# Optimization experiments

Measured on AMD Instinct MI355X. Metric: run time of the kernel, lower is better.

## Reference

```python
import jax, jax.numpy as jnp
import numpy as np

WS = 8          # window size
NH = 16         # num heads
EPS = 1e-6      # LinearAttention eps

def _rel_pos_index(ws):
    coords = np.stack(np.meshgrid(np.arange(ws), np.arange(ws), indexing='ij'))
    cf = coords.reshape(2, -1)
    rel = (cf[:, :, None] - cf[:, None, :]).transpose(1, 2, 0).astype(np.int64)
    rel[:, :, 0] += ws - 1
    rel[:, :, 1] += ws - 1
    rel[:, :, 0] *= 2 * ws - 1
    return rel.sum(-1)

REL_IDX = _rel_pos_index(WS)  # (ws*ws, ws*ws) int index into bias table

def conv1x1(x, w, b=None):
    y = jnp.einsum('bchw,oc->bohw', x, w)
    return y if b is None else y + b[None, :, None, None]

def conv3x3(x, w):
    return jax.lax.conv_general_dilated(x, w, (1, 1), [(1, 1), (1, 1)],
        dimension_numbers=('NCHW', 'OIHW', 'NCHW'))

def dwconv(x, w, pad):
    return jax.lax.conv_general_dilated(x, w, (1, 1), [(pad, pad), (pad, pad)],
        dimension_numbers=('NCHW', 'OIHW', 'NCHW'), feature_group_count=x.shape[1])

def bn(x, scale, bias):
    # eval-mode BatchNorm folded to per-channel affine (running_mean=0, running_var=1)
    return x * scale[None, :, None, None] + bias[None, :, None, None]

def rpad(x, l, r, t, b):
    return jnp.pad(x, ((0, 0), (0, 0), (t, b), (l, r)), mode='reflect')

def avgpool(x, kh, kw, ph, pw):
    # torch AvgPool2d with zero padding, count_include_pad=True
    xp = jnp.pad(x, ((0, 0), (0, 0), (ph, ph), (pw, pw)))
    s = jax.lax.reduce_window(xp, 0.0, jax.lax.add, (1, 1, kh, kw), (1, 1, 1, 1), 'VALID')
    return s / (kh * kw)

def linear_attention(x, gamma, wq, bq, wk, bk, wv, bv):
    B, C, H, W = x.shape
    N = H * W
    Q = conv1x1(x, wq, bq).reshape(B, -1, N)   # (B, M, N), M = C // 8
    K = conv1x1(x, wk, bk).reshape(B, -1, N)
    V = conv1x1(x, wv, bv).reshape(B, C, N)
    Q = Q / jnp.linalg.norm(Q, axis=-2, keepdims=True)  # l2_norm over channel dim
    K = K / jnp.linalg.norm(K, axis=-2, keepdims=True)
    tailor = 1.0 / (N + jnp.einsum('bmn,bm->bn', Q, K.sum(-1) + EPS))  # (B, N)
    vsum = V.sum(-1)                                    # (B, C)
    matrix = jnp.einsum('bmn,bcn->bmc', K, V)           # (B, M, C)
    msum = vsum[:, :, None] + jnp.einsum('bmn,bmc->bcn', Q, matrix)    # (B, C, N)
    return x + gamma * (msum * tailor[:, None, :]).reshape(B, C, H, W)

def fusion_attention(x, y, wqkv, wl1, s1, b1, wl2, s2, b2, rel, wdw, sp, bp, wpw):
    B, C, H, W = x.shape  # H, W divisible by WS -> pad() branch is a no-op
    local = bn(conv1x1(y, wl2), s2, b2) + bn(conv3x3(y, wl1), s1, b1)
    d = C // NH
    qkv = conv1x1(x, wqkv)                              # (B, 3C, H, W)
    hh, ww = H // WS, W // WS
    t = qkv.reshape(B, 3, NH, d, hh, WS, ww, WS)
    t = t.transpose(1, 0, 4, 6, 2, 5, 7, 3).reshape(3, B * hh * ww, NH, WS * WS, d)
    q, k, v = t[0], t[1], t[2]
    dots = jnp.einsum('wnqd,wnkd->wnqk', q, k) * (d ** -0.5)
    bias = rel[REL_IDX.reshape(-1)].reshape(WS * WS, WS * WS, NH).transpose(2, 0, 1)
    attn = jax.nn.softmax(dots + bias[None], axis=-1)
    out = jnp.einsum('wnqk,wnkd->wnqd', attn, v)
    out = out.reshape(B, hh, ww, NH, WS, WS, d).transpose(0, 3, 6, 1, 4, 2, 5).reshape(B, C, H, W)
    out = (avgpool(rpad(out, 0, 0, 0, 1), WS, 1, WS // 2 - 1, 0)
           + avgpool(rpad(out, 0, 1, 0, 0), 1, WS, 0, WS // 2 - 1))
    out = out + local
    out = rpad(out, 0, 1, 0, 1)                          # pad_out
    out = conv1x1(bn(dwconv(out, wdw, (WS - 1) // 2), sp, bp), wpw)  # SeparableConvBN
    return out[:, :, :H, :W]

def setup_inputs() -> dict:
    key = jax.random.key(0)
    ks = jax.random.split(key, 24)
    B, C, H, W = 2, 256, 256, 256
    M = C // 8
    n = jax.random.normal
    inp = {
        'x': n(ks[0], (B, C, H, W), jnp.float32),
        'y': n(ks[1], (B, C, H, W), jnp.float32),
        'la_gamma': jnp.float32(0.5),
        'la_wq': n(ks[2], (M, C)) * 0.05, 'la_bq': n(ks[3], (M,)) * 0.02,
        'la_wk': n(ks[4], (M, C)) * 0.05, 'la_bk': n(ks[5], (M,)) * 0.02,
        'la_wv': n(ks[6], (C, C)) * 0.05, 'la_bv': n(ks[7], (C,)) * 0.02,
        'fa_wqkv': n(ks[8], (3 * C, C)) * 0.05,
        'fa_wl1': n(ks[9], (C, C, 3, 3)) * 0.02,
        'fa_s1': 1.0 + n(ks[10], (C,)) * 0.02, 'fa_b1': n(ks[11], (C,)) * 0.02,
        'fa_wl2': n(ks[12], (C, C)) * 0.05,
        'fa_s2': 1.0 + n(ks[13], (C,)) * 0.02, 'fa_b2': n(ks[14], (C,)) * 0.02,
        'fa_rel': n(ks[15], ((2 * WS - 1) ** 2, NH)) * 0.02,
        'fa_wdw': n(ks[16], (C, 1, WS, WS)) * 0.05,
        'fa_sp': 1.0 + n(ks[17], (C,)) * 0.02, 'fa_bp': n(ks[18], (C,)) * 0.02,
        'fa_wpw': n(ks[19], (C, C)) * 0.05,
    }
    return inp

def reference(x, y, la_gamma, la_wq, la_bq, la_wk, la_bk, la_wv, la_bv,
              fa_wqkv, fa_wl1, fa_s1, fa_b1, fa_wl2, fa_s2, fa_b2,
              fa_rel, fa_wdw, fa_sp, fa_bp, fa_wpw):
    z = linear_attention(x, la_gamma, la_wq, la_bq, la_wk, la_bk, la_wv, la_bv)
    return fusion_attention(z, y, fa_wqkv, fa_wl1, fa_s1, fa_b1, fa_wl2, fa_s2, fa_b2,
                            fa_rel, fa_wdw, fa_sp, fa_bp, fa_wpw)
```

## Files before the change

kernel.cpp:

```cpp
#include <hip/hip_runtime.h>
#include <hip/hip_bf16.h>

#define DI __device__ __forceinline__

constexpr int Bc = 2, Cc = 256, Hc = 256, Wc = 256, Nc = Hc * Wc;
constexpr float LA_EPS = 1e-6f;

typedef __attribute__((ext_vector_type(8))) short short8;
typedef __attribute__((ext_vector_type(4))) float floatx4;
typedef __attribute__((ext_vector_type(16))) float floatx16;

union Frag { short8 v; uint u[4]; };

DI ushort f2bf(float f) {
    uint u = __float_as_uint(f);
    uint r = (u + 0x7fff + ((u >> 16) & 1)) >> 16;
    return (ushort)r;
}

DI float bf2f(ushort u) { return __uint_as_float((uint)u << 16); }

DI uint pack2(float a, float b) {
    return (uint)f2bf(a) | ((uint)f2bf(b) << 16);
}

DI void gload16(const void* g, void* l) {
    __builtin_amdgcn_global_load_lds(
        (const __attribute__((address_space(1))) void*)g,
        (__attribute__((address_space(3))) void*)l, 16, 0, 0);
}

__global__ __launch_bounds__(256) void kprep_x(const float* __restrict__ x,
        ushort* __restrict__ xbf)
{
    int blk = blockIdx.x;
    int b = blk >> 13;
    int rest = blk & 8191;
    int ci0 = (rest & 7) * 32;
    int n0 = (rest >> 3) * 64;
    int t = threadIdx.x;
    __shared__ uint u[16][65];
    int px = t & 63, cig = t >> 6;
    const float* yb = x + (((size_t)(b * 256 + ci0 + cig * 8)) << 16) + n0 + px;
    #pragma unroll
    for (int jj = 0; jj < 4; ++jj) {
        float v0 = yb[((size_t)(jj * 2)) << 16];
        float v1 = yb[((size_t)(jj * 2 + 1)) << 16];
        u[cig * 4 + jj][px] = pack2(v0, v1);
    }
    __syncthreads();
    uint* out32 = (uint*)xbf;
    int pr = t & 15, pg = t >> 4;
    #pragma unroll
    for (int g2 = 0; g2 < 4; ++g2) {
        int ppx = g2 * 16 + pg;
        size_t uidx = (((size_t)(b * 65536 + n0 + ppx) * 256 + ci0) >> 1) + pr;
        out32[uidx] = u[pr][ppx];
    }
}

__global__ __launch_bounds__(256) void kprep_qk(const float* __restrict__ wq,
        const float* __restrict__ wk, ushort* __restrict__ Wqkb)
{
    int idx = blockIdx.x * 256 + threadIdx.x;
    int oc = idx >> 8, ci = idx & 255;
    float v = (oc < 32) ? wq[oc * 256 + ci] : wk[(oc - 32) * 256 + ci];
    Wqkb[idx] = f2bf(v);
}

__global__ __launch_bounds__(512, 2) void k1_mfma(
        const ushort* __restrict__ xbf, const ushort* __restrict__ Wqkb,
        const float* __restrict__ bq, const float* __restrict__ bk,
        float* __restrict__ Qo, float* __restrict__ Ko)
{
    int blk = blockIdx.x;
    int b = blk >> 10;
    int px0 = (blk & 1023) << 6;
    int t = threadIdx.x;
    int lane = t & 63, w = t >> 6;
    int wr = w >> 2;
    int wc = w & 3;

    __shared__ ushort sW[64 * 256];
    __shared__ ushort sX[64 * 256];

    #pragma unroll
    for (int p = 0; p < 4; ++p) {
        int m = p * 512 + t;
        int row = m >> 5, ch = m & 31;
        const ushort* g = Wqkb + row * 256 + ((ch ^ (row & 7)) << 3);
        gload16(g, (char*)sW + p * 8192 + w * 1024);
    }
    const ushort* xb = xbf + (size_t)(b * 65536 + px0) * 256;
    #pragma unroll
    for (int p = 0; p < 4; ++p) {
        int m = p * 512 + t;
        int row = m >> 5, ch = m & 31;
        const ushort* g = xb + row * 256 + ((ch ^ (row & 7)) << 3);
        gload16(g, (char*)sX + p * 8192 + w * 1024);
    }
    __syncthreads();

    int l15 = lane & 15, l4 = lane >> 4;
    floatx4 acc[2];
    acc[0] = {0.f, 0.f, 0.f, 0.f};
    acc[1] = {0.f, 0.f, 0.f, 0.f};

    #pragma unroll
    for (int ks = 0; ks < 8; ++ks) {
        int cidx = ks * 4 + l4;
        short8 af[2];
        #pragma unroll
        for (int m2 = 0; m2 < 2; ++m2) {
            int row = wr * 32 + m2 * 16 + l15;
            af[m2] = *(const short8*)((const char*)sW + row * 512 + ((cidx ^ (row & 7)) << 4));
        }
        int brow = wc * 16 + l15;
        short8 bf_ = *(const short8*)((const char*)sX + brow * 512 + ((cidx ^ (brow & 7)) << 4));
        #pragma unroll
        for (int m2 = 0; m2 < 2; ++m2)
            acc[m2] = __builtin_amdgcn_mfma_f32_16x16x32_bf16(af[m2], bf_, acc[m2], 0, 0, 0);
    }

    const float* bias = wr ? bk : bq;
    float* outp = wr ? Ko : Qo;
    float v[2][4];
    float s = 0.f;
    #pragma unroll
    for (int m2 = 0; m2 < 2; ++m2)
        #pragma unroll
        for (int r = 0; r < 4; ++r) {
            float vv = acc[m2][r] + bias[m2 * 16 + l4 * 4 + r];
            v[m2][r] = vv;
            s += vv * vv;
        }
    s += __shfl_xor(s, 16);
    s += __shfl_xor(s, 32);
    float rn = rsqrtf(s);
    int px = px0 + wc * 16 + l15;
    #pragma unroll
    for (int m2 = 0; m2 < 2; ++m2)
        #pragma unroll
        for (int r = 0; r < 4; ++r) {
            int oc = m2 * 16 + l4 * 4 + r;
            outp[((size_t)(b * 32 + oc) << 16) + px] = v[m2][r] * rn;
        }
}

__global__ __launch_bounds__(256) void k2_kx(const ushort* __restrict__ xbf,
        const float* __restrict__ Kn, float* __restrict__ KXp,
        float* __restrict__ xsp, float* __restrict__ ksp)
{
    int blk = blockIdx.x;
    int b = blk >> 9;
    int blkl = blk & 511;
    int t = threadIdx.x;
    int n0 = blkl * 128;
    __shared__ float kT[32][128];
    for (int i = t; i < 4096; i += 256) {
        int m = i >> 7, p = i & 127;
        kT[m][p] = Kn[((size_t)(b * 32 + m) << 16) + n0 + p];
    }
    __syncthreads();
    float acc[32];
    #pragma unroll
    for (int m = 0; m < 32; ++m) acc[m] = 0.f;
    float xs = 0.f;
    const ushort* xb = xbf + (((size_t)(b * 65536 + n0)) << 8) + t;
    for (int p4 = 0; p4 < 32; ++p4) {
        float xv0 = bf2f(xb[(size_t)(p4 * 4 + 0) << 8]);
        float xv1 = bf2f(xb[(size_t)(p4 * 4 + 1) << 8]);
        float xv2 = bf2f(xb[(size_t)(p4 * 4 + 2) << 8]);
        float xv3 = bf2f(xb[(size_t)(p4 * 4 + 3) << 8]);
        xs += xv0 + xv1 + xv2 + xv3;
        #pragma unroll
        for (int m = 0; m < 32; ++m) {
            floatx4 kv = *(const floatx4*)&kT[m][p4 * 4];
            acc[m] += kv[0] * xv0 + kv[1] * xv1 + kv[2] * xv2 + kv[3] * xv3;
        }
    }
    xsp[blk * 256 + t] = xs;
    if (t < 32) {
        float ks = 0.f;
        for (int p = 0; p < 128; ++p) ks += kT[t][p];
        ksp[blk * 32 + t] = ks;
    }
    #pragma unroll
    for (int m = 0; m < 32; ++m) KXp[(size_t)blk * 8192 + m * 256 + t] = acc[m];
}

__global__ __launch_bounds__(256) void k2r(const float* __restrict__ KXp,
        const float* __restrict__ xsp, const float* __restrict__ ksp,
        float* __restrict__ KX, float* __restrict__ xsum, float* __restrict__ Ksum)
{
    int blk = blockIdx.x, t = threadIdx.x;
    if (blk < 64) {
        int gidx = blk * 256 + t;
        int b = gidx >> 13, idx = gidx & 8191;
        float s = 0.f;
        for (int ch = 0; ch < 512; ++ch)
            s += KXp[(size_t)((b << 9) + ch) * 8192 + idx];
        KX[gidx] = s;
    } else if (blk < 66) {
        int b = blk - 64;
        float s = 0.f;
        for (int ch = 0; ch < 512; ++ch)
            s += xsp[((b << 9) + ch) * 256 + t];
        xsum[b * 256 + t] = s;
    } else {
        int b = blk - 66;
        if (t < 32) {
            float s = 0.f;
            for (int ch = 0; ch < 512; ++ch)
                s += ksp[((b << 9) + ch) * 32 + t];
            Ksum[b * 32 + t] = s;
        }
    }
}

__global__ __launch_bounds__(256) void k3_mat(const float* __restrict__ wv,
        const float* __restrict__ bv, const float* __restrict__ KX,
        const float* __restrict__ xsum, const float* __restrict__ Ksum,
        float* __restrict__ matrix, float* __restrict__ vsum)
{
    int b = blockIdx.x, t = threadIdx.x;
    __shared__ float sx[256];
    __shared__ float sk[32];
    __shared__ float skx[32][256];
    __shared__ float wT[256][65];
    sx[t] = xsum[b * 256 + t];
    if (t < 32) sk[t] = Ksum[b * 32 + t];
    for (int j = 0; j < 32; ++j) skx[j][t] = KX[(b * 32 + j) * 256 + t];
    float vs = bv[t] * (float)Nc;
    float mv[32];
    #pragma unroll
    for (int m = 0; m < 32; ++m) mv[m] = 0.f;
    for (int cc0 = 0; cc0 < 256; cc0 += 64) {
        __syncthreads();
        for (int i = 0; i < 64; ++i) {
            int c = i * 4 + (t >> 6);
            wT[c][t & 63] = wv[(size_t)c * 256 + cc0 + (t & 63)];
        }
        __syncthreads();
        for (int ccl = 0; ccl < 64; ++ccl) {
            float w = wT[t][ccl];
            int cc = cc0 + ccl;
            vs += w * sx[cc];
            #pragma unroll
            for (int m = 0; m < 32; ++m) mv[m] += w * skx[m][cc];
        }
    }
    vsum[b * 256 + t] = vs;
    float bvt = bv[t];
    for (int m = 0; m < 32; ++m) matrix[(b * 32 + m) * 256 + t] = mv[m] + bvt * sk[m];
}

__global__ __launch_bounds__(256) void k4_z(const float* __restrict__ x,
        const float* __restrict__ Q, const float* __restrict__ matrix,
        const float* __restrict__ vsum, const float* __restrict__ Ksum,
        const float* __restrict__ gamma_p, ushort* __restrict__ zbf)
{
    int b = blockIdx.x >> 10;
    int n0 = (blockIdx.x & 1023) * 64;
    int t = threadIdx.x;
    int px = t & 63, g = t >> 6;
    __shared__ float qT[32][64];
    __shared__ float mat[32][256];
    __shared__ float vs[256];
    __shared__ float tail[64];
    __shared__ float sk[32];
    __shared__ uint zsh[64 * 128];
    #pragma unroll
    for (int j = 0; j < 8; ++j) {
        int m = j * 4 + g;
        qT[m][px] = Q[((size_t)b * 32 + m) * Nc + n0 + px];
    }
    for (int j = 0; j < 32; ++j) {
        int idx = j * 256 + t;
        (&mat[0][0])[idx] = matrix[b * 8192 + idx];
    }
    vs[t] = vsum[b * 256 + t];
    if (t < 32) sk[t] = Ksum[b * 32 + t] + LA_EPS;
    __syncthreads();
    if (t < 64) {
        float s = 0.f;
        #pragma unroll
        for (int m = 0; m < 32; ++m) s += qT[m][t] * sk[m];
        tail[t] = 1.0f / ((float)Nc + s);
    }
    __syncthreads();
    float gamma = gamma_p[0];
    float tl = tail[px];
    for (int l = 0; l < 64; l += 2) {
        int c0 = g * 64 + l;
        float s0 = vs[c0], s1 = vs[c0 + 1];
        #pragma unroll
        for (int m = 0; m < 32; ++m) {
            float qv = qT[m][px];
            s0 += qv * mat[m][c0];
            s1 += qv * mat[m][c0 + 1];
        }
        size_t idx0 = (size_t)(b * 256 + c0) * Nc + n0 + px;
        float z0 = x[idx0] + gamma * s0 * tl;
        float z1 = x[idx0 + Nc] + gamma * s1 * tl;
        int cp = c0 >> 1;
        zsh[(px * 512 + (((cp >> 2) ^ (px & 7)) << 4) + (cp & 3) * 4) >> 2] = pack2(z0, z1);
    }
    __syncthreads();
    const uint4* zl = (const uint4*)zsh;
    uint4* gz = (uint4*)(zbf + (((size_t)(b * 65536 + n0)) << 8));
    #pragma unroll
    for (int i2 = 0; i2 < 8; ++i2)
        gz[i2 * 256 + t] = zl[i2 * 256 + t];
}

__global__ __launch_bounds__(256) void kprep_y(const float* __restrict__ y,
        ushort* __restrict__ ybf)
{
    int blk = blockIdx.x;
    int b = blk >> 13;
    int rest = blk & 8191;
    int ci0 = (rest & 7) * 32;
    int n0 = (rest >> 3) * 64;
    int row = n0 >> 8, x = n0 & 255;
    int t = threadIdx.x;
    __shared__ uint u[16][65];
    int px = t & 63, cig = t >> 6;
    const float* yb = y + (((size_t)(b * 256 + ci0 + cig * 8)) << 16) + n0 + px;
    #pragma unroll
    for (int jj = 0; jj < 4; ++jj) {
        float v0 = yb[((size_t)(jj * 2)) << 16];
        float v1 = yb[((size_t)(jj * 2 + 1)) << 16];
        u[cig * 4 + jj][px] = pack2(v0, v1);
    }
    __syncthreads();
    uint* out32 = (uint*)ybf;
    size_t pbase = (size_t)(row + 1) * 258 + (x + 1);
    int pr = t & 15, pg = t >> 4;
    #pragma unroll
    for (int g2 = 0; g2 < 4; ++g2) {
        int ppx = g2 * 16 + pg;
        size_t uidx = (((size_t)b * 258 * 258 * 256 + (pbase + ppx) * 256 + ci0) >> 1) + pr;
        out32[uidx] = u[pr][ppx];
    }
}

__global__ __launch_bounds__(256) void kprep_w(const float* __restrict__ wl1,
        const float* __restrict__ s1, const float* __restrict__ wl2,
        const float* __restrict__ s2, ushort* __restrict__ Wb)
{
    int idx = blockIdx.x * 256 + threadIdx.x;
    int tp = idx >> 16;
    int r = idx & 65535;
    int co = r >> 8;
    float v = wl1[(size_t)r * 9 + tp] * s1[co];
    if (tp == 4) v += wl2[r] * s2[co];
    Wb[idx] = f2bf(v);
}

__global__ __launch_bounds__(256) void kprep_qw(const float* __restrict__ wqkv,
        ushort* __restrict__ Wqb)
{
    int idx = blockIdx.x * 256 + threadIdx.x;
    float v = wqkv[idx];
    if (idx < 65536) v *= 0.25f;
    Wqb[idx] = f2bf(v);
}

__global__ __launch_bounds__(256) void kprep_pw(const float* __restrict__ wpw,
        ushort* __restrict__ Wpwb)
{
    int idx = blockIdx.x * 256 + threadIdx.x;
    Wpwb[idx] = f2bf(wpw[idx]);
}

__global__ __launch_bounds__(256) void kprep_rel(const float* __restrict__ rel,
        ushort* __restrict__ relbf)
{
    int idx = blockIdx.x * 256 + threadIdx.x;
    if (idx < 3600) {
        int d = idx >> 4, h = idx & 15;
        relbf[h * 226 + d] = f2bf(rel[idx]);
    }
}

__global__ __launch_bounds__(512, 2) void k5_mfma(
        const ushort* __restrict__ ybf, const ushort* __restrict__ Wb,
        const float* __restrict__ b1, const float* __restrict__ b2,
        ushort* __restrict__ L)
{
    int blk = blockIdx.x;
    int b = blk >> 9;
    int y0 = (blk >> 1) & 255;
    int x0 = (blk & 1) << 7;
    int t = threadIdx.x;
    int lane = t & 63;
    int w = t >> 6;
    int wr = w >> 1;
    int wc = w & 1;

    __shared__ ushort sW[256 * 64];
    __shared__ ushort sY[128 * 64];

    floatx4 acc[4][4];
    #pragma unroll
    for (int m = 0; m < 4; ++m)
        #pragma unroll
        for (int n = 0; n < 4; ++n)
            acc[m][n] = {0.f, 0.f, 0.f, 0.f};

    const ushort* yb = ybf + (size_t)b * 258 * 258 * 256;
    int ldsWbase = w * 64 * 16;
    int ldsYbase = w * 64 * 16;

    for (int tp = 0; tp < 9; ++tp) {
        int dy = tp / 3 - 1, dx = tp % 3 - 1;
        const ushort* yrow = yb + ((size_t)(y0 + dy + 1) * 258 + (x0 + dx + 1)) * 256;
        const ushort* wtap = Wb + tp * 65536;
        for (int cb = 0; cb < 4; ++cb) {
            int ci0 = cb * 64;
            __syncthreads();
            #pragma unroll
            for (int p = 0; p < 4; ++p) {
                int m = p * 512 + t;
                int row = m >> 3, ch = m & 7;
                const ushort* g = wtap + row * 256 + ci0 + ((ch ^ (row & 7)) << 3);
                gload16(g, (char*)sW + p * 512 * 16 + ldsWbase);
            }
            #pragma unroll
            for (int p = 0; p < 2; ++p) {
                int m = p * 512 + t;
                int pxr = m >> 3, ch = m & 7;
                const ushort* g = yrow + (size_t)pxr * 256 + ci0 + ((ch ^ (pxr & 7)) << 3);
                gload16(g, (char*)sY + p * 512 * 16 + ldsYbase);
            }
            __syncthreads();
            #pragma unroll
            for (int kk = 0; kk < 2; ++kk) {
                int chunkb = kk * 4 + (lane >> 4);
                short8 afr[4];
                #pragma unroll
                for (int m2 = 0; m2 < 4; ++m2) {
                    int row = wr * 64 + m2 * 16 + (lane & 15);
                    int ch = chunkb ^ (row & 7);
                    afr[m2] = *(const short8*)((const char*)sW + row * 128 + ch * 16);
                }
                #pragma unroll
                for (int n2 = 0; n2 < 4; ++n2) {
                    int row = wc * 64 + n2 * 16 + (lane & 15);
                    int ch = chunkb ^ (row & 7);
                    short8 bfr = *(const short8*)((const char*)sY + row * 128 + ch * 16);
                    #pragma unroll
                    for (int m2 = 0; m2 < 4; ++m2)
                        acc[m2][n2] = __builtin_amdgcn_mfma_f32_16x16x32_bf16(
                            afr[m2], bfr, acc[m2][n2], 0, 0, 0);
                }
            }
        }
    }
    int pxb = x0 + wc * 64 + (lane & 15);
    #pragma unroll
    for (int m2 = 0; m2 < 4; ++m2) {
        int cobase = wr * 64 + m2 * 16 + (lane >> 4) * 4;
        #pragma unroll
        for (int r = 0; r < 4; ++r) {
            int co = cobase + r;
            float bias = b1[co] + b2[co];
            ushort* dst = L + (((size_t)(b * 256 + co)) << 16) + y0 * 256 + pxb;
            #pragma unroll
            for (int n2 = 0; n2 < 4; ++n2)
                dst[n2 * 16] = f2bf(acc[m2][n2][r] + bias);
        }
    }
}

__global__ __launch_bounds__(512, 2) void k6_mfma(const ushort* __restrict__ zbf,
        const ushort* __restrict__ Wqb, const ushort* __restrict__ relbf,
        float* __restrict__ A)
{
    int blk = blockIdx.x;
    int wxp = blk & 15, wy = (blk >> 4) & 31, b = blk >> 9;
    int t = threadIdx.x;
    int lane = t & 63;
    int w = t >> 6;
    int win = w >> 2;
    int wq4 = w & 3;

    __shared__ ushort zT[128 * 256];
    __shared__ ushort srel[16 * 226];

    char* zTc = (char*)zT;

    {
        const ushort* zb = zbf + (((size_t)b) << 16) * 256;
        #pragma unroll
        for (int p = 0; p < 8; ++p) {
            int m = p * 512 + t;
            int row = m >> 5, ch = m & 31;
            int win2 = row >> 6, px = row & 63;
            int gy = wy * 8 + (px >> 3);
            int gx = (wxp * 2 + win2) * 8 + (px & 7);
            const ushort* g = zb + (((size_t)(gy * 256 + gx)) << 8) + ch * 8;
            gload16(g, zTc + p * 8192 + w * 1024);
        }
    }
    for (int i = t; i < 16 * 226; i += 512) srel[i] = relbf[i];
    __syncthreads();

    int l15 = lane & 15, l4 = lane >> 4;
    int l31 = lane & 31, l5 = lane >> 5;
    bool hilane = (l5 != 0);
    bool hi16 = (l31 & 16) != 0;
    int srcA = (l5 << 5) + (l31 & 15);
    int srcB = srcA + 16;
    int pxbase = win * 64;

    for (int hrep = 0; hrep < 4; ++hrep) {
        int h = wq4 * 4 + hrep;
        const ushort* srh = &srel[h * 226];

        floatx4 qacc[4] = {}, kacc[4] = {}, vacc[4] = {};
        #pragma unroll
        for (int ks = 0; ks < 8; ++ks) {
            short8 awq = *(const short8*)(Wqb + ((h * 16 + l15) << 8) + ks * 32 + (l4 << 3));
            short8 awk = *(const short8*)(Wqb + ((256 + h * 16 + l15) << 8) + ks * 32 + (l4 << 3));
            short8 bwv = *(const short8*)(Wqb + ((512 + h * 16 + l15) << 8) + ks * 32 + (l4 << 3));
            #pragma unroll
            for (int n = 0; n < 4; ++n) {
                int px = n * 16 + l15;
                short8 bz = *(const short8*)(zTc + (pxbase + px) * 512 + (((ks * 4 + l4) ^ (px & 7)) << 4));
                qacc[n] = __builtin_amdgcn_mfma_f32_16x16x32_bf16(awq, bz, qacc[n], 0, 0, 0);
                kacc[n] = __builtin_amdgcn_mfma_f32_16x16x32_bf16(awk, bz, kacc[n], 0, 0, 0);
                vacc[n] = __builtin_amdgcn_mfma_f32_16x16x32_bf16(bz, bwv, vacc[n], 0, 0, 0);
            }
        }

        Frag bq[2];
        {
            uint plo[4], phi[4];
            #pragma unroll
            for (int n = 0; n < 4; ++n) {
                plo[n] = pack2(qacc[n][0], qacc[n][1]);
                phi[n] = pack2(qacc[n][2], qacc[n][3]);
            }
            #pragma unroll
            for (int it = 0; it < 2; ++it) {
                uint a0 = (uint)__shfl((int)plo[it * 2], srcA), a1 = (uint)__shfl((int)plo[it * 2 + 1], srcA);
                uint b0 = (uint)__shfl((int)phi[it * 2], srcA), b1 = (uint)__shfl((int)phi[it * 2 + 1], srcA);
                uint c0 = (uint)__shfl((int)plo[it * 2], srcB), c1 = (uint)__shfl((int)plo[it * 2 + 1], srcB);
                uint d0 = (uint)__shfl((int)phi[it * 2], srcB), d1 = (uint)__shfl((int)phi[it * 2 + 1], srcB);
                bq[it].u[0] = hi16 ? a1 : a0;
                bq[it].u[1] = hi16 ? b1 : b0;
                bq[it].u[2] = hi16 ? c1 : c0;
                bq[it].u[3] = hi16 ? d1 : d0;
            }
        }
        Frag ak[2];
        {
            uint plo[4], phi[4];
            #pragma unroll
            for (int n = 0; n < 4; ++n) {
                plo[n] = pack2(kacc[n][0], kacc[n][1]);
                phi[n] = pack2(kacc[n][2], kacc[n][3]);
            }
            #pragma unroll
            for (int jt = 0; jt < 2; ++jt) {
                uint a0 = (uint)__shfl((int)plo[jt * 2], srcA), a1 = (uint)__shfl((int)plo[jt * 2 + 1], srcA);
                uint b0 = (uint)__shfl((int)phi[jt * 2], srcA), b1 = (uint)__shfl((int)phi[jt * 2 + 1], srcA);
                uint c0 = (uint)__shfl((int)plo[jt * 2], srcB), c1 = (uint)__shfl((int)plo[jt * 2 + 1], srcB);
                uint d0 = (uint)__shfl((int)phi[jt * 2], srcB), d1 = (uint)__shfl((int)phi[jt * 2 + 1], srcB);
                ak[jt].u[0] = hi16 ? a1 : a0;
                ak[jt].u[1] = hi16 ? b1 : b0;
                ak[jt].u[2] = hi16 ? c1 : c0;
                ak[jt].u[3] = hi16 ? d1 : d0;
            }
        }
        Frag av[4];
        {
            uint v01[4], v23[4];
            #pragma unroll
            for (int m = 0; m < 4; ++m) {
                v01[m] = pack2(vacc[m][0], vacc[m][1]);
                v23[m] = pack2(vacc[m][2], vacc[m][3]);
            }
            #pragma unroll
            for (int jc = 0; jc < 4; ++jc) {
                av[jc].u[0] = (uint)__shfl((int)v01[jc], srcA);
                av[jc].u[1] = (uint)__shfl((int)v23[jc], srcA);
                av[jc].u[2] = (uint)__shfl((int)v01[jc], srcB);
                av[jc].u[3] = (uint)__shfl((int)v23[jc], srcB);
            }
        }

        #pragma unroll
        for (int it = 0; it < 2; ++it) {
            floatx16 st[2];
            #pragma unroll
            for (int jt = 0; jt < 2; ++jt) {
                floatx16 zc = {};
                st[jt] = __builtin_amdgcn_mfma_f32_32x32x16_bf16(ak[jt].v, bq[it].v, zc, 0, 0, 0);
            }
            int i = it * 32 + l31;
            int Ai = (i >> 3) * 15 + (i & 7) + 112;
            float mx = -1e30f;
            #pragma unroll
            for (int jt = 0; jt < 2; ++jt)
                #pragma unroll
                for (int r = 0; r < 16; ++r) {
                    int j = jt * 32 + (r & 3) + 8 * (r >> 2) + 4 * l5;
                    int Bjr = (j >> 3) * 15 + (j & 7);
                    float s = st[jt][r] + bf2f(srh[Ai - Bjr]);
                    st[jt][r] = s;
                    mx = fmaxf(mx, s);
                }
            mx = fmaxf(mx, __shfl_xor(mx, 32));
            float sum = 0.f;
            #pragma unroll
            for (int jt = 0; jt < 2; ++jt)
                #pragma unroll
                for (int r = 0; r < 16; ++r) {
                    float e = __expf(st[jt][r] - mx);
                    st[jt][r] = e;
                    sum += e;
                }
            sum += __shfl_xor(sum, 32);
            float rinv = 1.0f / sum;

            floatx16 ot = {};
            #pragma unroll
            for (int jc = 0; jc < 4; ++jc) {
                int jt = jc >> 1, rb = (jc & 1) * 8;
                uint u0 = pack2(st[jt][rb + 0], st[jt][rb + 1]);
                uint u1 = pack2(st[jt][rb + 2], st[jt][rb + 3]);
                uint u2 = pack2(st[jt][rb + 4], st[jt][rb + 5]);
                uint u3 = pack2(st[jt][rb + 6], st[jt][rb + 7]);
                uint s0 = (uint)__shfl_xor((int)u0, 32);
                uint s1 = (uint)__shfl_xor((int)u1, 32);
                uint s2 = (uint)__shfl_xor((int)u2, 32);
                uint s3 = (uint)__shfl_xor((int)u3, 32);
                Frag bf;
                bf.u[0] = hilane ? s2 : u0;
                bf.u[1] = hilane ? s3 : u1;
                bf.u[2] = hilane ? u2 : s0;
                bf.u[3] = hilane ? u3 : s1;
                ot = __builtin_amdgcn_mfma_f32_32x32x16_bf16(av[jc].v, bf.v, ot, 0, 0, 0);
            }
            int gy = wy * 8 + (i >> 3);
            int gx = (wxp * 2 + win) * 8 + (i & 7);
            float* Ab = A + (((size_t)(b * 256 + h * 16)) << 16) + gy * 256 + gx;
            #pragma unroll
            for (int r = 0; r < 8; ++r) {
                int d = (r & 3) + 8 * (r >> 2) + 4 * l5;
                Ab[(size_t)d << 16] = ot[r] * rinv;
            }
        }
    }
}

__global__ __launch_bounds__(256) void k7_pool(const float* __restrict__ A,
        ushort* __restrict__ L)
{
    int blk = blockIdx.x;
    int tile = blk & 15;
    int c = (blk >> 4) & 255;
    int b = blk >> 12;
    int ty = (tile >> 2) * 64, tx = (tile & 3) * 64;
    int t = threadIdx.x;
    __shared__ float aT[71][73];
    const float* Ac = A + ((size_t)(b * 256 + c) << 16);
    for (int i = t; i < 71 * 71; i += 256) {
        int rr = i / 71, cc = i - rr * 71;
        int gy = ty + rr - 3, gx = tx + cc - 3;
        float v = 0.f;
        if (gy >= 0 && gy <= 256 && gx >= 0 && gx <= 256) {
            int ry = (gy == 256) ? 254 : gy;
            int rx = (gx == 256) ? 254 : gx;
            v = Ac[ry * 256 + rx];
        }
        aT[rr][cc] = v;
    }
    __syncthreads();
    int jj = t & 63;
    int oy0 = (t >> 6) * 16;
    ushort* Lc = L + ((size_t)(b * 256 + c) << 16);
    #pragma unroll 4
    for (int dy = 0; dy < 16; ++dy) {
        int oi = oy0 + dy;
        float sv = 0.f, sh = 0.f;
        #pragma unroll
        for (int u = 0; u < 8; ++u) {
            sv += aT[oi + u][jj + 3];
            sh += aT[oi + 3][jj + u];
        }
        int idx = (ty + oi) * 256 + tx + jj;
        Lc[idx] = f2bf(bf2f(Lc[idx]) + 0.125f * (sv + sh));
    }
}

__global__ __launch_bounds__(256) void k8_dw(const ushort* __restrict__ P,
        const float* __restrict__ wdw, const float* __restrict__ sp,
        const float* __restrict__ bp, ushort* __restrict__ D)
{
    int blk = blockIdx.x;
    int tile = blk & 63;
    int c = (blk >> 6) & 255;
    int b = blk >> 14;
    int ty = (tile >> 3) * 32, tx = (tile & 7) * 32;
    int t = threadIdx.x;
    __shared__ float pT[39][40];
    __shared__ float wT[64];
    const ushort* Pc = P + ((size_t)(b * 256 + c) << 16);
    for (int i = t; i < 39 * 40; i += 256) {
        int rr = i / 40, cc = i - rr * 40;
        int gy = ty + rr - 3, gx = tx + cc - 3;
        float v = 0.f;
        if (gy >= 0 && gy <= 256 && gx >= 0 && gx <= 256) {
            int ry = (gy == 256) ? 254 : gy;
            int rx = (gx == 256) ? 254 : gx;
            v = bf2f(Pc[ry * 256 + rx]);
        }
        pT[rr][cc] = v;
    }
    if (t < 64) wT[t] = wdw[c * 64 + t];
    __syncthreads();
    int jj = t & 31;
    int oy0 = (t >> 5) * 4;
    float acc[4] = {0.f, 0.f, 0.f, 0.f};
    #pragma unroll
    for (int r = 0; r < 11; ++r) {
        float pv[8];
        #pragma unroll
        for (int v = 0; v < 8; ++v) pv[v] = pT[oy0 + r][jj + v];
        #pragma unroll
        for (int dy = 0; dy < 4; ++dy) {
            if (dy >= r - 7 && dy <= r && dy <= 3) {
                int u = r - dy;
                #pragma unroll
                for (int v = 0; v < 8; ++v)
                    acc[dy] += wT[u * 8 + v] * pv[v];
            }
        }
    }
    float spc = sp[c], bpc = bp[c];
    ushort* Dc = D + ((size_t)(b * 256 + c) << 16);
    #pragma unroll
    for (int dy = 0; dy < 4; ++dy)
        Dc[(ty + oy0 + dy) * 256 + tx + jj] = f2bf(spc * acc[dy] + bpc);
}

__global__ __launch_bounds__(512, 2) void k9_mfma(
        const ushort* __restrict__ D, const ushort* __restrict__ Wpwb,
        float* __restrict__ out)
{
    int blk = blockIdx.x;
    int b = blk >> 9;
    int px0 = (blk & 511) << 7;
    int t = threadIdx.x;
    int lane = t & 63;
    int w = t >> 6;
    int wr = w >> 1, wc = w & 1;

    __shared__ ushort sW[256 * 64];
    __shared__ ushort sD[128 * 64];

    floatx4 acc[4][4];
    #pragma unroll
    for (int m = 0; m < 4; ++m)
        #pragma unroll
        for (int n = 0; n < 4; ++n)
            acc[m][n] = {0.f, 0.f, 0.f, 0.f};

    int ldsWbase = w * 64 * 16;

    for (int cb = 0; cb < 4; ++cb) {
        int ci0 = cb * 64;
        __syncthreads();
        #pragma unroll
        for (int p = 0; p < 4; ++p) {
            int m = p * 512 + t;
            int row = m >> 3, ch = m & 7;
            const ushort* g = Wpwb + row * 256 + ci0 + ((ch ^ (row & 7)) << 3);
            gload16(g, (char*)sW + p * 512 * 16 + ldsWbase);
        }
        #pragma unroll
        for (int p = 0; p < 2; ++p) {
            int m = p * 512 + t;
            int ci = m & 63, pxb = (m >> 6) * 8;
            short8 v = *(const short8*)(D + ((size_t)(b * 256 + ci0 + ci) << 16) + px0 + pxb);
            #pragma unroll
            for (int k2 = 0; k2 < 8; ++k2) {
                int px = pxb + k2;
                *(ushort*)((char*)sD + px * 128 + (((ci >> 3) ^ (px & 7)) << 4) + (ci & 7) * 2) =
                    (ushort)v[k2];
            }
        }
        __syncthreads();
        #pragma unroll
        for (int kk = 0; kk < 2; ++kk) {
            int chunkb = kk * 4 + (lane >> 4);
            short8 afr[4];
            #pragma unroll
            for (int m2 = 0; m2 < 4; ++m2) {
                int row = wr * 64 + m2 * 16 + (lane & 15);
                int ch = chunkb ^ (row & 7);
                afr[m2] = *(const short8*)((const char*)sW + row * 128 + ch * 16);
            }
            #pragma unroll
            for (int n2 = 0; n2 < 4; ++n2) {
                int row = wc * 64 + n2 * 16 + (lane & 15);
                int ch = chunkb ^ (row & 7);
                short8 bfr = *(const short8*)((const char*)sD + row * 128 + ch * 16);
                #pragma unroll
                for (int m2 = 0; m2 < 4; ++m2)
                    acc[m2][n2] = __builtin_amdgcn_mfma_f32_16x16x32_bf16(
                        afr[m2], bfr, acc[m2][n2], 0, 0, 0);
            }
        }
    }
    int pxb = px0 + wc * 64 + (lane & 15);
    #pragma unroll
    for (int m2 = 0; m2 < 4; ++m2) {
        int cobase = wr * 64 + m2 * 16 + (lane >> 4) * 4;
        #pragma unroll
        for (int r = 0; r < 4; ++r) {
            int co = cobase + r;
            float* dst = out + (((size_t)(b * 256 + co)) << 16) + pxb;
            #pragma unroll
            for (int n2 = 0; n2 < 4; ++n2)
                dst[n2 * 16] = acc[m2][n2][r];
        }
    }
}

extern "C" void kernel_launch(void* const* d_in, const int* in_sizes, int n_in,
                              void* d_out, int out_size, void* d_ws, size_t ws_size,
                              hipStream_t stream)
{
    (void)in_sizes; (void)n_in; (void)out_size; (void)ws_size;
    const float* x     = (const float*)d_in[0];
    const float* y     = (const float*)d_in[1];
    const float* gamma = (const float*)d_in[2];
    const float* la_wq = (const float*)d_in[3];
    const float* la_bq = (const float*)d_in[4];
    const float* la_wk = (const float*)d_in[5];
    const float* la_bk = (const float*)d_in[6];
    const float* la_wv = (const float*)d_in[7];
    const float* la_bv = (const float*)d_in[8];
    const float* wqkv  = (const float*)d_in[9];
    const float* wl1   = (const float*)d_in[10];
    const float* s1    = (const float*)d_in[11];
    const float* b1    = (const float*)d_in[12];
    const float* wl2   = (const float*)d_in[13];
    const float* s2    = (const float*)d_in[14];
    const float* b2    = (const float*)d_in[15];
    const float* rel   = (const float*)d_in[16];
    const float* wdw   = (const float*)d_in[17];
    const float* sp    = (const float*)d_in[18];
    const float* bp    = (const float*)d_in[19];
    const float* wpw   = (const float*)d_in[20];
    float* out = (float*)d_out;

    float* ws = (float*)d_ws;
    float* Q      = ws;
    float* Kn     = ws + 4194304;
    float* stats  = ws + 8388608;
    float* Ksum   = stats;
    float* xsum   = stats + 64;
    float* KX     = stats + 576;
    float* matrix = stats + 16960;
    float* vsum   = stats + 33344;
    float* A      = ws + 8429568;
    float* L      = A + 33554432;

    float* KXp   = L;
    float* xsp   = L + 8388608;
    float* ksp   = L + 8650752;
    ushort* xbf  = (ushort*)(L + 8683520);
    ushort* Wqkb = (ushort*)(L + 25460736);

    ushort* Wb    = (ushort*)Kn;
    ushort* Wqb   = (ushort*)Kn + 600064;
    ushort* Wpwb  = (ushort*)Kn + 798720;
    ushort* relbf = (ushort*)Kn + 864256;
    ushort* ybf   = (ushort*)A;
    ushort* Dbf   = (ushort*)A;
    ushort* zbf   = (ushort*)d_out;
    ushort* Lb    = (ushort*)L;

    hipMemsetAsync(ybf, 0, (size_t)2 * 258 * 258 * 256 * sizeof(ushort), stream);

    kprep_y  <<<16384, 256, 0, stream>>>(y, ybf);
    kprep_x  <<<16384, 256, 0, stream>>>(x, xbf);
    kprep_qk <<<64,    256, 0, stream>>>(la_wq, la_wk, Wqkb);
    k1_mfma  <<<2048,  512, 0, stream>>>(xbf, Wqkb, la_bq, la_bk, Q, Kn);
    k2_kx    <<<1024,  256, 0, stream>>>(xbf, Kn, KXp, xsp, ksp);
    kprep_w  <<<2304,  256, 0, stream>>>(wl1, s1, wl2, s2, Wb);
    kprep_qw <<<768,   256, 0, stream>>>(wqkv, Wqb);
    kprep_pw <<<256,   256, 0, stream>>>(wpw, Wpwb);
    kprep_rel<<<15,    256, 0, stream>>>(rel, relbf);
    k2r      <<<68,    256, 0, stream>>>(KXp, xsp, ksp, KX, xsum, Ksum);
    k3_mat   <<<2,     256, 0, stream>>>(la_wv, la_bv, KX, xsum, Ksum, matrix, vsum);
    k4_z     <<<2048,  256, 0, stream>>>(x, Q, matrix, vsum, Ksum, gamma, zbf);
    k5_mfma  <<<1024,  512, 0, stream>>>(ybf, Wb, b1, b2, Lb);
    k6_mfma  <<<1024,  512, 0, stream>>>(zbf, Wqb, relbf, A);
    k7_pool  <<<8192,  256, 0, stream>>>(A, Lb);
    k8_dw    <<<32768, 256, 0, stream>>>(Lb, wdw, sp, bp, Dbf);
    k9_mfma  <<<1024,  512, 0, stream>>>(Dbf, Wpwb, out);
}
```

Before: 1.046 ms.

## Fuse strip-pool add and depthwise conv into one tiled kernel

Merges the pooling kernel, which added the strip average pool of the attention output into the bf16 local tensor, with the depthwise 8x8 conv kernel. Each 64x64 tile now loads a haloed attention tile, computes the pooled-plus-local values for a 74x74 halo region in shared memory, and runs the depthwise conv from there. This removes the bf16 round-trip write and reread of the intermediate and one launch. In exchange it recomputes pooling on halo pixels, uses much more shared memory per block (lower occupancy), and keeps 16 accumulators per thread. The output buffer moves to a separate region.

```diff
diff --git a/kernel.cpp b/kernel.cpp
--- a/kernel.cpp
+++ b/kernel.cpp
@@ -657,8 +657,10 @@
     }
 }
 
-__global__ __launch_bounds__(256) void k7_pool(const float* __restrict__ A,
-        ushort* __restrict__ L)
+__global__ __launch_bounds__(256) void k78_pooldw(const float* __restrict__ A,
+        const ushort* __restrict__ Lc, const float* __restrict__ wdw,
+        const float* __restrict__ sp, const float* __restrict__ bp,
+        ushort* __restrict__ D)
 {
     int blk = blockIdx.x;
     int tile = blk & 15;
@@ -666,75 +668,62 @@
     int b = blk >> 12;
     int ty = (tile >> 2) * 64, tx = (tile & 3) * 64;
     int t = threadIdx.x;
-    __shared__ float aT[71][73];
+
+    __shared__ float aT[81][84];
+    __shared__ float lT[74][76];
+    __shared__ float wT[64];
+
     const float* Ac = A + ((size_t)(b * 256 + c) << 16);
-    for (int i = t; i < 71 * 71; i += 256) {
-        int rr = i / 71, cc = i - rr * 71;
-        int gy = ty + rr - 3, gx = tx + cc - 3;
+    const ushort* Lcc = Lc + ((size_t)(b * 256 + c) << 16);
+
+    for (int i = t; i < 81 * 81; i += 256) {
+        int a = i / 81, bc = i - a * 81;
+        int rr = ty - 6 + a, cc = tx - 6 + bc;
         float v = 0.f;
+        if (rr >= 0 && rr <= 256 && cc >= 0 && cc <= 256) {
+            int mr = (rr == 256) ? 254 : rr;
+            int mc = (cc == 256) ? 254 : cc;
+            v = Ac[mr * 256 + mc];
+        }
+        aT[a][bc] = v;
+    }
+    if (t < 64) wT[t] = wdw[c * 64 + t];
+    __syncthreads();
+
+    for (int i = t; i < 74 * 74; i += 256) {
+        int a = i / 74, bc = i - a * 74;
+        int gy = ty - 3 + a, gx = tx - 3 + bc;
+        float L = 0.f;
         if (gy >= 0 && gy <= 256 && gx >= 0 && gx <= 256) {
-            int ry = (gy == 256) ? 254 : gy;
-            int rx = (gx == 256) ? 254 : gx;
-            v = Ac[ry * 256 + rx];
-        }
-        aT[rr][cc] = v;
-    }
-    __syncthreads();
+            int my = (gy == 256) ? 254 : gy;
+            int mx = (gx == 256) ? 254 : gx;
+            int ar = my - ty + 6, ac = mx - tx + 6;
+            float sv = 0.f, sh = 0.f;
+            #pragma unroll
+            for (int u = 0; u < 8; ++u) {
+                sv += aT[ar - 3 + u][ac];
+                sh += aT[ar][ac - 3 + u];
+            }
+            L = bf2f(Lcc[my * 256 + mx]) + 0.125f * (sv + sh);
+        }
+        lT[a][bc] = L;
+    }
+    __syncthreads();
+
     int jj = t & 63;
     int oy0 = (t >> 6) * 16;
-    ushort* Lc = L + ((size_t)(b * 256 + c) << 16);
-    #pragma unroll 4
-    for (int dy = 0; dy < 16; ++dy) {
-        int oi = oy0 + dy;
-        float sv = 0.f, sh = 0.f;
-        #pragma unroll
-        for (int u = 0; u < 8; ++u) {
-            sv += aT[oi + u][jj + 3];
-            sh += aT[oi + 3][jj + u];
-        }
-        int idx = (ty + oi) * 256 + tx + jj;
-        Lc[idx] = f2bf(bf2f(Lc[idx]) + 0.125f * (sv + sh));
-    }
-}
-
-__global__ __launch_bounds__(256) void k8_dw(const ushort* __restrict__ P,
-        const float* __restrict__ wdw, const float* __restrict__ sp,
-        const float* __restrict__ bp, ushort* __restrict__ D)
-{
-    int blk = blockIdx.x;
-    int tile = blk & 63;
-    int c = (blk >> 6) & 255;
-    int b = blk >> 14;
-    int ty = (tile >> 3) * 32, tx = (tile & 7) * 32;
-    int t = threadIdx.x;
-    __shared__ float pT[39][40];
-    __shared__ float wT[64];
-    const ushort* Pc = P + ((size_t)(b * 256 + c) << 16);
-    for (int i = t; i < 39 * 40; i += 256) {
-        int rr = i / 40, cc = i - rr * 40;
-        int gy = ty + rr - 3, gx = tx + cc - 3;
-        float v = 0.f;
-        if (gy >= 0 && gy <= 256 && gx >= 0 && gx <= 256) {
-            int ry = (gy == 256) ? 254 : gy;
-            int rx = (gx == 256) ? 254 : gx;
-            v = bf2f(Pc[ry * 256 + rx]);
-        }
-        pT[rr][cc] = v;
-    }
-    if (t < 64) wT[t] = wdw[c * 64 + t];
-    __syncthreads();
-    int jj = t & 31;
-    int oy0 = (t >> 5) * 4;
-    float acc[4] = {0.f, 0.f, 0.f, 0.f};
-    #pragma unroll
-    for (int r = 0; r < 11; ++r) {
+    float acc[16];
+    #pragma unroll
+    for (int dy = 0; dy < 16; ++dy) acc[dy] = 0.f;
+    #pragma unroll
+    for (int rr = 0; rr < 23; ++rr) {
         float pv[8];
         #pragma unroll
-        for (int v = 0; v < 8; ++v) pv[v] = pT[oy0 + r][jj + v];
-        #pragma unroll
-        for (int dy = 0; dy < 4; ++dy) {
-            if (dy >= r - 7 && dy <= r && dy <= 3) {
-                int u = r - dy;
+        for (int v = 0; v < 8; ++v) pv[v] = lT[oy0 + rr][jj + v];
+        #pragma unroll
+        for (int dy = 0; dy < 16; ++dy) {
+            if (dy >= rr - 7 && dy <= rr && dy <= 15) {
+                int u = rr - dy;
                 #pragma unroll
                 for (int v = 0; v < 8; ++v)
                     acc[dy] += wT[u * 8 + v] * pv[v];
@@ -744,7 +733,7 @@
     float spc = sp[c], bpc = bp[c];
     ushort* Dc = D + ((size_t)(b * 256 + c) << 16);
     #pragma unroll
-    for (int dy = 0; dy < 4; ++dy)
+    for (int dy = 0; dy < 16; ++dy)
         Dc[(ty + oy0 + dy) * 256 + tx + jj] = f2bf(spc * acc[dy] + bpc);
 }
 
@@ -883,9 +872,9 @@
     ushort* Wpwb  = (ushort*)Kn + 798720;
     ushort* relbf = (ushort*)Kn + 864256;
     ushort* ybf   = (ushort*)A;
-    ushort* Dbf   = (ushort*)A;
     ushort* zbf   = (ushort*)d_out;
     ushort* Lb    = (ushort*)L;
+    ushort* Dbf   = (ushort*)L + 33554432;
 
     hipMemsetAsync(ybf, 0, (size_t)2 * 258 * 258 * 256 * sizeof(ushort), stream);
 
@@ -903,7 +892,6 @@
     k4_z     <<<2048,  256, 0, stream>>>(x, Q, matrix, vsum, Ksum, gamma, zbf);
     k5_mfma  <<<1024,  512, 0, stream>>>(ybf, Wb, b1, b2, Lb);
     k6_mfma  <<<1024,  512, 0, stream>>>(zbf, Wqb, relbf, A);
-    k7_pool  <<<8192,  256, 0, stream>>>(A, Lb);
-    k8_dw    <<<32768, 256, 0, stream>>>(Lb, wdw, sp, bp, Dbf);
+    k78_pooldw<<<8192, 256, 0, stream>>>(A, Lb, wdw, sp, bp, Dbf);
     k9_mfma  <<<1024,  512, 0, stream>>>(Dbf, Wpwb, out);
 }
```

New measurement: 1.240 ms. 1.19x slower.
